# Performance work log

Hardware: AMD Instinct MI355X
Metric: run time of the kernel (lower is better)

The kernel has to match this reference:

```python
import jax, jax.numpy as jnp
import numpy as np

B, S, D, H = 2, 2048, 1024, 16
HD = D // H  # 64


def rotate_half(x):
    x1, x2 = x[..., : x.shape[-1] // 2], x[..., x.shape[-1] // 2 :]
    return jnp.concatenate((-x2, x1), axis=-1)


def setup_inputs() -> dict:
    key = jax.random.key(0)
    ks = jax.random.split(key, 8)
    return {
        "hidden_states": jax.random.normal(ks[0], (B, S, D), jnp.float32),
        "attention_bias": jax.random.normal(ks[1], (B, 1, S, S), jnp.float32),
        "cos": jax.random.uniform(ks[2], (1, S, 1, HD), jnp.float32),
        "sin": jax.random.uniform(ks[3], (1, S, 1, HD), jnp.float32),
        "Wqkv": jax.random.normal(ks[4], (D, 3 * D), jnp.float32) * (D ** -0.5),
        "bqkv": jnp.zeros((3 * D,), jnp.float32),
        "Wo": jax.random.normal(ks[5], (D, D), jnp.float32) * (D ** -0.5),
        "bo": jnp.zeros((D,), jnp.float32),
    }


def reference(hidden_states, attention_bias, cos, sin, Wqkv, bqkv, Wo, bo):
    # packed QKV projection: [B,S,D] -> [B,S,3D]
    qkv = hidden_states @ Wqkv + bqkv
    q, k, v = jnp.split(qkv, 3, axis=-1)
    # reshape to [B,S,H,HD]
    q = q.reshape(B, S, H, HD)
    k = k.reshape(B, S, H, HD)
    v = v.reshape(B, S, H, HD)
    # rotary position embedding
    q = q * cos + rotate_half(q) * sin
    k = k * cos + rotate_half(k) * sin
    # scaled dot-product attention with additive bias
    scores = jnp.einsum("bqhd,bkhd->bhqk", q, k) / jnp.sqrt(jnp.float32(HD))
    scores = scores + attention_bias
    probs = jax.nn.softmax(scores, axis=-1)
    ctx = jnp.einsum("bhqk,bkhd->bqhd", probs, v)  # [B,S,H,HD]
    ctx = ctx.reshape(B, S, D)
    return ctx @ Wo + bo
```

## Files before the change

### kernel.cpp

```cpp
#include <hip/hip_runtime.h>
#include <stdint.h>

typedef unsigned short u16;
typedef __attribute__((ext_vector_type(8))) short short8;
typedef __attribute__((ext_vector_type(4))) float f32x4;

#define DI __device__ __forceinline__

constexpr int S_LEN = 2048;
constexpr float LOG2E = 1.44269504088896f;
constexpr float SC = 0.125f * 1.44269504088896f;

DI float bf2f(u16 u) { union { uint32_t i; float f; } v; v.i = ((uint32_t)u) << 16; return v.f; }
DI u16 f2bf(float f) {
  union { float f; uint32_t i; } v; v.f = f;
  return (u16)((v.i + 0x7FFFu + ((v.i >> 16) & 1u)) >> 16);
}
DI uint32_t cvtpk(float lo, float hi) {
  uint32_t r;
  asm("v_cvt_pk_bf16_f32 %0, %1, %2" : "=v"(r) : "v"(lo), "v"(hi));
  return r;
}
DI float exp2r(float x) {
  float r;
  asm("v_exp_f32 %0, %1" : "=v"(r) : "v"(x));
  return r;
}

DI void cp16(const void* g, void* l) {
  auto gp = reinterpret_cast<const __attribute__((address_space(1))) uint32_t*>(
      reinterpret_cast<uintptr_t>(g));
  auto lp = reinterpret_cast<__attribute__((address_space(3))) uint32_t*>(
      reinterpret_cast<uintptr_t>(l));
  __builtin_amdgcn_global_load_lds(gp, lp, 16, 0, 0);
}

DI f32x4 mfma16(short8 a, short8 b, f32x4 c) {
  return __builtin_amdgcn_mfma_f32_16x16x32_bf16(a, b, c, 0, 0, 0);
}

DI int permk(int rl) {
  return ((rl >> 5) & 1) * 32 + ((rl >> 2) & 3) * 8 + ((rl >> 4) & 1) * 4 + (rl & 3);
}

__global__ __launch_bounds__(256) void k_cvt(const float* __restrict__ in,
                                             u16* __restrict__ out, int n4) {
  int i = blockIdx.x * 256 + threadIdx.x;
  if (i >= n4) return;
  float4 v = ((const float4*)in)[i];
  ushort4 o = { f2bf(v.x), f2bf(v.y), f2bf(v.z), f2bf(v.w) };
  ((ushort4*)out)[i] = o;
}

__global__ __launch_bounds__(256) void k_cvtb(const float* __restrict__ in,
                                              u16* __restrict__ out, int n4) {
  int i = blockIdx.x * 256 + threadIdx.x;
  if (i >= n4) return;
  float4 v = ((const float4*)in)[i];
  ushort4 o = { f2bf(v.x * LOG2E), f2bf(v.y * LOG2E), f2bf(v.z * LOG2E), f2bf(v.w * LOG2E) };
  ((ushort4*)out)[i] = o;
}

__global__ __launch_bounds__(256) void k_tr(const float* __restrict__ in,
                                            u16* __restrict__ out, int R, int C) {
  __shared__ float t[32][33];
  int tx = threadIdx.x & 31, ty = threadIdx.x >> 5;
  int c0 = blockIdx.x * 32, r0 = blockIdx.y * 32;
#pragma unroll
  for (int k = 0; k < 4; k++)
    t[ty + 8 * k][tx] = in[(size_t)(r0 + ty + 8 * k) * C + c0 + tx];
  __syncthreads();
#pragma unroll
  for (int k = 0; k < 4; k++)
    out[(size_t)(c0 + ty + 8 * k) * R + r0 + tx] = f2bf(t[tx][ty + 8 * k]);
}

template <int STORE_F32>
__global__ __launch_bounds__(256) void k_gemm(const u16* __restrict__ A,
                                              const u16* __restrict__ Bt,
                                              const float* __restrict__ bias,
                                              void* __restrict__ Cout,
                                              int N, int K, int nbx) {
  __shared__ u16 Al[128 * 32];
  __shared__ u16 Bl[128 * 32];
  int nwg = gridDim.x;
  int per = nwg >> 3;
  int id = blockIdx.x;
  int sid = (id & 7) * per + (id >> 3);
  int bx = sid % nbx, by = sid / nbx;
  int row0 = by * 128, col0 = bx * 128;
  int tid = threadIdx.x;
  int lane = tid & 63, wave = tid >> 6;
  int lg = lane >> 4, lc = lane & 15;
  int wr = wave >> 1, wc = wave & 1;
  int srow = tid >> 2, sseg = tid & 3;
  const u16* ga = A + (size_t)(row0 + srow) * K + sseg * 8;
  const u16* gb = Bt + (size_t)(col0 + srow) * K + sseg * 8;
  u16* la = Al + tid * 8;
  u16* lb = Bl + tid * 8;
  size_t half = (size_t)64 * K;
  f32x4 acc[4][4] = {};
  for (int ko = 0; ko < K; ko += 32) {
    cp16(ga + ko, la);
    cp16(ga + ko + half, la + 2048);
    cp16(gb + ko, lb);
    cp16(gb + ko + half, lb + 2048);
    __syncthreads();
    short8 af[4], bf[4];
#pragma unroll
    for (int i = 0; i < 4; i++)
      af[i] = *(const short8*)&Al[(wr * 64 + i * 16 + lc) * 32 + lg * 8];
#pragma unroll
    for (int j = 0; j < 4; j++)
      bf[j] = *(const short8*)&Bl[(wc * 64 + j * 16 + lc) * 32 + lg * 8];
#pragma unroll
    for (int i = 0; i < 4; i++)
#pragma unroll
      for (int j = 0; j < 4; j++) acc[i][j] = mfma16(af[i], bf[j], acc[i][j]);
    __syncthreads();
  }
#pragma unroll
  for (int i = 0; i < 4; i++) {
    int r = row0 + wr * 64 + i * 16 + lg * 4;
#pragma unroll
    for (int j = 0; j < 4; j++) {
      int c = col0 + wc * 64 + j * 16 + lc;
      float bv = bias[c];
#pragma unroll
      for (int q = 0; q < 4; q++) {
        float v = acc[i][j][q] + bv;
        if constexpr (STORE_F32)
          ((float*)Cout)[(size_t)(r + q) * N + c] = v;
        else
          ((u16*)Cout)[(size_t)(r + q) * N + c] = f2bf(v);
      }
    }
  }
}

__global__ __launch_bounds__(256) void k_rope(u16* __restrict__ qkv,
                                              const float* __restrict__ cosb,
                                              const float* __restrict__ sinb) {
  int idx = blockIdx.x * 256 + threadIdx.x;
  int d = idx & 31;
  int h = (idx >> 5) & 15;
  int s = (idx >> 9) & 2047;
  int b = idx >> 20;
  size_t base = (size_t)(b * S_LEN + s) * 3072 + h * 64 + d;
  float c1 = cosb[s * 64 + d], s1 = sinb[s * 64 + d];
  float c2 = cosb[s * 64 + d + 32], s2 = sinb[s * 64 + d + 32];
  float x1 = bf2f(qkv[base]), x2 = bf2f(qkv[base + 32]);
  qkv[base] = f2bf(x1 * c1 - x2 * s1);
  qkv[base + 32] = f2bf(x2 * c2 + x1 * s2);
  float y1 = bf2f(qkv[base + 1024]), y2 = bf2f(qkv[base + 1056]);
  qkv[base + 1024] = f2bf(y1 * c1 - y2 * s1);
  qkv[base + 1056] = f2bf(y2 * c2 + y1 * s2);
}

__global__ __launch_bounds__(256) void k_vtrans(const u16* __restrict__ qkv,
                                                u16* __restrict__ vtg) {
  __shared__ u16 Vl[64 * 66];
  int bh = blockIdx.y, b = bh >> 4, h = bh & 15;
  int s0 = blockIdx.x * 64;
  int tid = threadIdx.x;
  int r = tid >> 3, seg = tid & 7;
  const u16* src = qkv + (size_t)(b * S_LEN + s0) * 3072 + 2048 + h * 64 + seg * 8;
#pragma unroll
  for (int p = 0; p < 2; p++) {
    int s = r + 32 * p;
    short8 v = *(const short8*)(src + (size_t)s * 3072);
    const uint32_t* vw = (const uint32_t*)&v;
    uint32_t* dst = (uint32_t*)&Vl[s * 66 + seg * 8];
#pragma unroll
    for (int q = 0; q < 4; q++) dst[q] = vw[q];
  }
  __syncthreads();
  u16* out = vtg + (size_t)bh * 64 * 2048 + s0 + seg * 8;
#pragma unroll
  for (int p = 0; p < 2; p++) {
    int d = r + 32 * p;
    short8 o;
#pragma unroll
    for (int j = 0; j < 8; j++) o[j] = (short)Vl[(seg * 8 + j) * 66 + d];
    *(short8*)(out + (size_t)d * 2048) = o;
  }
}

DI float sm_pa(const f32x4 st[4], const short8* bc, short8 pa[2]) {
  float acc = 0.f;
  uint32_t w[4][2];
#pragma unroll
  for (int j = 0; j < 4; j++) {
    int base = (j & 1) * 4;
    float b0 = bf2f((u16)(j < 2 ? bc[0][base + 0] : bc[1][base + 0]));
    float b1 = bf2f((u16)(j < 2 ? bc[0][base + 1] : bc[1][base + 1]));
    float b2 = bf2f((u16)(j < 2 ? bc[0][base + 2] : bc[1][base + 2]));
    float b3 = bf2f((u16)(j < 2 ? bc[0][base + 3] : bc[1][base + 3]));
    float e0 = exp2r(st[j][0] * SC + b0);
    float e1 = exp2r(st[j][1] * SC + b1);
    float e2 = exp2r(st[j][2] * SC + b2);
    float e3 = exp2r(st[j][3] * SC + b3);
    acc += (e0 + e1) + (e2 + e3);
    w[j][0] = cvtpk(e0, e1);
    w[j][1] = cvtpk(e2, e3);
  }
  union { short8 s; uint32_t u[4]; } p0, p1;
  p0.u[0] = w[0][0]; p0.u[1] = w[0][1]; p0.u[2] = w[1][0]; p0.u[3] = w[1][1];
  p1.u[0] = w[2][0]; p1.u[1] = w[2][1]; p1.u[2] = w[3][0]; p1.u[3] = w[3][1];
  pa[0] = p0.s;
  pa[1] = p1.s;
  return acc;
}

DI void attn_store(u16* __restrict__ ctx, const f32x4 o[4], float lsumT,
                   size_t rowbase, int hcol, int lg, int lc) {
  float rinv[4];
#pragma unroll
  for (int r = 0; r < 4; r++) rinv[r] = 1.0f / __shfl(lsumT, lg * 4 + r);
#pragma unroll
  for (int j = 0; j < 4; j++)
#pragma unroll
    for (int r = 0; r < 4; r++)
      ctx[(rowbase + lg * 4 + r) * 1024 + hcol + j * 16 + lc] =
          f2bf(o[j][r] * rinv[r]);
}

__global__ __launch_bounds__(256, 2) void k_attn(const u16* __restrict__ qkv,
                                                 const u16* __restrict__ biasl2,
                                                 const u16* __restrict__ vtg,
                                                 u16* __restrict__ ctx) {
  __shared__ u16 Kl[2][4096];
  __shared__ u16 Vl[2][4096];
  constexpr int nkt = 32;
  int id = blockIdx.x;
  int idx = id >> 3;
  int bh = (id & 7) * 4 + (idx & 3);
  int qt = idx >> 2;
  int b = bh >> 4, h = bh & 15;
  int tid = threadIdx.x, lane = tid & 63, wave = tid >> 6;
  int lg = lane >> 4, lc = lane & 15;
  int q0 = qt * 128 + wave * 32;

  const u16* qb = qkv + (size_t)(b * S_LEN + q0 + lc) * 3072 + h * 64 + lg * 8;
  short8 qf[2][2];
#pragma unroll
  for (int s = 0; s < 2; s++) {
    qf[s][0] = *(const short8*)(qb + (size_t)s * 16 * 3072);
    qf[s][1] = *(const short8*)(qb + (size_t)s * 16 * 3072 + 32);
  }

  int srow = tid >> 3, sseg = tid & 7;
  const u16* kst[2];
  const u16* vst[2];
#pragma unroll
  for (int p = 0; p < 2; p++) {
    int rl = srow + 32 * p;
    int sw = (sseg ^ (rl & 7)) * 8;
    kst[p] = qkv + (size_t)(b * S_LEN + permk(rl)) * 3072 + 1024 + h * 64 + sw;
    vst[p] = vtg + (size_t)bh * 64 * 2048 + (size_t)rl * 2048 + sw;
  }

  const u16* bp0 = biasl2 + ((size_t)b * S_LEN + q0 + lc) * 2048 + lg * 8;
  const u16* bp1 = bp0 + (size_t)16 * 2048;

  f32x4 o0[4] = {}, o1[4] = {};
  float lsum0 = 0.f, lsum1 = 0.f;

#pragma unroll
  for (int p = 0; p < 2; p++) {
    cp16(kst[p], (u16*)&Kl[0][0] + p * 2048 + tid * 8);
    cp16(vst[p], (u16*)&Vl[0][0] + p * 2048 + tid * 8);
    kst[p] += (size_t)64 * 3072;
    vst[p] += 64;
  }
  short8 bA[4], bB[4];
  bA[0] = *(const short8*)bp0;
  bA[1] = *(const short8*)(bp0 + 32);
  bA[2] = *(const short8*)bp1;
  bA[3] = *(const short8*)(bp1 + 32);
  bp0 += 64;
  bp1 += 64;
  __syncthreads();

  auto tile = [&](int kt, int cur, const short8* bc, short8* bn) {
    if (kt < nkt - 1) {
#pragma unroll
      for (int p = 0; p < 2; p++) {
        cp16(kst[p], (u16*)&Kl[cur ^ 1][0] + p * 2048 + tid * 8);
        cp16(vst[p], (u16*)&Vl[cur ^ 1][0] + p * 2048 + tid * 8);
        kst[p] += (size_t)64 * 3072;
        vst[p] += 64;
      }
      bn[0] = *(const short8*)bp0;
      bn[1] = *(const short8*)(bp0 + 32);
      bn[2] = *(const short8*)bp1;
      bn[3] = *(const short8*)(bp1 + 32);
      bp0 += 64;
      bp1 += 64;
    }
    f32x4 st0[4] = {}, st1[4] = {};
    __builtin_amdgcn_s_setprio(1);
#pragma unroll
    for (int kk = 0; kk < 2; kk++) {
      short8 kf[4];
#pragma unroll
      for (int j = 0; j < 4; j++) {
        int row = j * 16 + lc;
        kf[j] = *(const short8*)&Kl[cur][row * 64 + (((kk * 4 + lg) ^ (row & 7)) * 8)];
      }
#pragma unroll
      for (int j = 0; j < 4; j++) {
        st0[j] = mfma16(kf[j], qf[0][kk], st0[j]);
        st1[j] = mfma16(kf[j], qf[1][kk], st1[j]);
      }
    }
    __builtin_amdgcn_s_setprio(0);
    short8 pa0[2], pa1[2];
    lsum0 += sm_pa(st0, bc, pa0);
    lsum1 += sm_pa(st1, bc + 2, pa1);
    __builtin_amdgcn_s_setprio(1);
#pragma unroll
    for (int kk = 0; kk < 2; kk++) {
      short8 vf[4];
#pragma unroll
      for (int j = 0; j < 4; j++) {
        int row = j * 16 + lc;
        vf[j] = *(const short8*)&Vl[cur][row * 64 + (((kk * 4 + lg) ^ (row & 7)) * 8)];
      }
#pragma unroll
      for (int j = 0; j < 4; j++) {
        o0[j] = mfma16(pa0[kk], vf[j], o0[j]);
        o1[j] = mfma16(pa1[kk], vf[j], o1[j]);
      }
    }
    __builtin_amdgcn_s_setprio(0);
    __syncthreads();
  };

  for (int kt = 0; kt < nkt; kt += 2) {
    tile(kt, 0, bA, bB);
    tile(kt + 1, 1, bB, bA);
  }

  float t0 = lsum0;
  t0 += __shfl_xor(t0, 16);
  t0 += __shfl_xor(t0, 32);
  float t1 = lsum1;
  t1 += __shfl_xor(t1, 16);
  t1 += __shfl_xor(t1, 32);
  size_t rowbase = (size_t)b * S_LEN + q0;
  attn_store(ctx, o0, t0, rowbase, h * 64, lg, lc);
  attn_store(ctx, o1, t1, rowbase + 16, h * 64, lg, lc);
}

extern "C" void kernel_launch(void* const* d_in, const int* in_sizes, int n_in,
                              void* d_out, int out_size, void* d_ws, size_t ws_size,
                              hipStream_t stream) {
  (void)in_sizes; (void)n_in; (void)out_size; (void)ws_size;
  const float* hs   = (const float*)d_in[0];
  const float* bias = (const float*)d_in[1];
  const float* cosb = (const float*)d_in[2];
  const float* sinb = (const float*)d_in[3];
  const float* Wqkv = (const float*)d_in[4];
  const float* bqkv = (const float*)d_in[5];
  const float* Wo   = (const float*)d_in[6];
  const float* bo   = (const float*)d_in[7];
  float* out = (float*)d_out;
  char* ws = (char*)d_ws;
  u16* h_bf   = (u16*)(ws + 0);
  u16* wqkvT  = (u16*)(ws + 8388608);
  u16* woT    = (u16*)(ws + 14680064);
  u16* biasbf = (u16*)(ws + 16777216);
  u16* qkv    = (u16*)(ws + 33554432);
  u16* vtg    = (u16*)(ws + 58720256);
  u16* ctxb   = (u16*)(ws + 67108864);

  k_cvt<<<4096, 256, 0, stream>>>(hs, h_bf, 1048576);
  k_cvtb<<<8192, 256, 0, stream>>>(bias, biasbf, 2097152);
  k_tr<<<dim3(96, 32), 256, 0, stream>>>(Wqkv, wqkvT, 1024, 3072);
  k_tr<<<dim3(32, 32), 256, 0, stream>>>(Wo, woT, 1024, 1024);
  k_gemm<0><<<768, 256, 0, stream>>>(h_bf, wqkvT, bqkv, qkv, 3072, 1024, 24);
  k_rope<<<8192, 256, 0, stream>>>(qkv, cosb, sinb);
  k_vtrans<<<dim3(32, 32), 256, 0, stream>>>(qkv, vtg);
  k_attn<<<512, 256, 0, stream>>>(qkv, biasbf, vtg, ctxb);
  k_gemm<1><<<256, 256, 0, stream>>>(ctxb, woT, bo, out, 1024, 1024, 8);
}
```

Baseline: 159.7 us.

## Fuse RoPE into QKV GEMM epilogue and halve attention query tile

Rotary embedding for the Q and K columns now runs inside the QKV GEMM epilogue. This drops the separate k_rope kernel and its read-modify-write pass over the bf16 qkv buffer, and applies RoPE to f32 values before the bf16 rounding. The attention kernel now gives each wave 16 query rows instead of 32. That doubles the grid to 1024 blocks and raises the launch-bounds occupancy hint from 2 to 4, to increase parallelism and cut register pressure. The cost is that each K/V tile staged in LDS is reused by half as many query rows, which doubles K/V traffic from global memory and L2.

```diff
diff --git a/kernel.cpp b/kernel.cpp
--- a/kernel.cpp
+++ b/kernel.cpp
@@ -75,11 +75,13 @@
     out[(size_t)(c0 + ty + 8 * k) * R + r0 + tx] = f2bf(t[tx][ty + 8 * k]);
 }
 
-template <int STORE_F32>
+template <int STORE_F32, int ROPE>
 __global__ __launch_bounds__(256) void k_gemm(const u16* __restrict__ A,
                                               const u16* __restrict__ Bt,
                                               const float* __restrict__ bias,
                                               void* __restrict__ Cout,
+                                              const float* __restrict__ cosb,
+                                              const float* __restrict__ sinb,
                                               int N, int K, int nbx) {
   __shared__ u16 Al[128 * 32];
   __shared__ u16 Bl[128 * 32];
@@ -119,42 +121,42 @@
       for (int j = 0; j < 4; j++) acc[i][j] = mfma16(af[i], bf[j], acc[i][j]);
     __syncthreads();
   }
+  int cbase = col0 + wc * 64 + lc;
+  float bv[4];
+#pragma unroll
+  for (int j = 0; j < 4; j++) bv[j] = bias[cbase + j * 16];
+  bool do_rope = false;
+  if constexpr (ROPE) do_rope = (col0 < 2048);
 #pragma unroll
   for (int i = 0; i < 4; i++) {
     int r = row0 + wr * 64 + i * 16 + lg * 4;
 #pragma unroll
-    for (int j = 0; j < 4; j++) {
-      int c = col0 + wc * 64 + j * 16 + lc;
-      float bv = bias[c];
-#pragma unroll
-      for (int q = 0; q < 4; q++) {
-        float v = acc[i][j][q] + bv;
+    for (int q = 0; q < 4; q++) {
+      float v[4];
+#pragma unroll
+      for (int j = 0; j < 4; j++) v[j] = acc[i][j][q] + bv[j];
+      if (do_rope) {
+        int s = (r + q) & 2047;
+        const float* cb = cosb + s * 64 + lc;
+        const float* sb = sinb + s * 64 + lc;
+#pragma unroll
+        for (int jp = 0; jp < 2; jp++) {
+          float cl = cb[jp * 16], sl = sb[jp * 16];
+          float ch = cb[jp * 16 + 32], sh = sb[jp * 16 + 32];
+          float x1 = v[jp], x2 = v[jp + 2];
+          v[jp] = x1 * cl - x2 * sl;
+          v[jp + 2] = x2 * ch + x1 * sh;
+        }
+      }
+#pragma unroll
+      for (int j = 0; j < 4; j++) {
         if constexpr (STORE_F32)
-          ((float*)Cout)[(size_t)(r + q) * N + c] = v;
+          ((float*)Cout)[(size_t)(r + q) * N + cbase + j * 16] = v[j];
         else
-          ((u16*)Cout)[(size_t)(r + q) * N + c] = f2bf(v);
+          ((u16*)Cout)[(size_t)(r + q) * N + cbase + j * 16] = f2bf(v[j]);
       }
     }
   }
-}
-
-__global__ __launch_bounds__(256) void k_rope(u16* __restrict__ qkv,
-                                              const float* __restrict__ cosb,
-                                              const float* __restrict__ sinb) {
-  int idx = blockIdx.x * 256 + threadIdx.x;
-  int d = idx & 31;
-  int h = (idx >> 5) & 15;
-  int s = (idx >> 9) & 2047;
-  int b = idx >> 20;
-  size_t base = (size_t)(b * S_LEN + s) * 3072 + h * 64 + d;
-  float c1 = cosb[s * 64 + d], s1 = sinb[s * 64 + d];
-  float c2 = cosb[s * 64 + d + 32], s2 = sinb[s * 64 + d + 32];
-  float x1 = bf2f(qkv[base]), x2 = bf2f(qkv[base + 32]);
-  qkv[base] = f2bf(x1 * c1 - x2 * s1);
-  qkv[base + 32] = f2bf(x2 * c2 + x1 * s2);
-  float y1 = bf2f(qkv[base + 1024]), y2 = bf2f(qkv[base + 1056]);
-  qkv[base + 1024] = f2bf(y1 * c1 - y2 * s1);
-  qkv[base + 1056] = f2bf(y2 * c2 + y1 * s2);
 }
 
 __global__ __launch_bounds__(256) void k_vtrans(const u16* __restrict__ qkv,
@@ -225,7 +227,7 @@
           f2bf(o[j][r] * rinv[r]);
 }
 
-__global__ __launch_bounds__(256, 2) void k_attn(const u16* __restrict__ qkv,
+__global__ __launch_bounds__(256, 4) void k_attn(const u16* __restrict__ qkv,
                                                  const u16* __restrict__ biasl2,
                                                  const u16* __restrict__ vtg,
                                                  u16* __restrict__ ctx) {
@@ -239,15 +241,11 @@
   int b = bh >> 4, h = bh & 15;
   int tid = threadIdx.x, lane = tid & 63, wave = tid >> 6;
   int lg = lane >> 4, lc = lane & 15;
-  int q0 = qt * 128 + wave * 32;
+  int q0 = qt * 64 + wave * 16;
 
   const u16* qb = qkv + (size_t)(b * S_LEN + q0 + lc) * 3072 + h * 64 + lg * 8;
-  short8 qf[2][2];
-#pragma unroll
-  for (int s = 0; s < 2; s++) {
-    qf[s][0] = *(const short8*)(qb + (size_t)s * 16 * 3072);
-    qf[s][1] = *(const short8*)(qb + (size_t)s * 16 * 3072 + 32);
-  }
+  short8 qf0 = *(const short8*)qb;
+  short8 qf1 = *(const short8*)(qb + 32);
 
   int srow = tid >> 3, sseg = tid & 7;
   const u16* kst[2];
@@ -260,11 +258,10 @@
     vst[p] = vtg + (size_t)bh * 64 * 2048 + (size_t)rl * 2048 + sw;
   }
 
-  const u16* bp0 = biasl2 + ((size_t)b * S_LEN + q0 + lc) * 2048 + lg * 8;
-  const u16* bp1 = bp0 + (size_t)16 * 2048;
-
-  f32x4 o0[4] = {}, o1[4] = {};
-  float lsum0 = 0.f, lsum1 = 0.f;
+  const u16* bp = biasl2 + ((size_t)b * S_LEN + q0 + lc) * 2048 + lg * 8;
+
+  f32x4 o[4] = {};
+  float lsum = 0.f;
 
 #pragma unroll
   for (int p = 0; p < 2; p++) {
@@ -273,13 +270,10 @@
     kst[p] += (size_t)64 * 3072;
     vst[p] += 64;
   }
-  short8 bA[4], bB[4];
-  bA[0] = *(const short8*)bp0;
-  bA[1] = *(const short8*)(bp0 + 32);
-  bA[2] = *(const short8*)bp1;
-  bA[3] = *(const short8*)(bp1 + 32);
-  bp0 += 64;
-  bp1 += 64;
+  short8 bA[2], bB[2];
+  bA[0] = *(const short8*)bp;
+  bA[1] = *(const short8*)(bp + 32);
+  bp += 64;
   __syncthreads();
 
   auto tile = [&](int kt, int cur, const short8* bc, short8* bn) {
@@ -291,46 +285,33 @@
         kst[p] += (size_t)64 * 3072;
         vst[p] += 64;
       }
-      bn[0] = *(const short8*)bp0;
-      bn[1] = *(const short8*)(bp0 + 32);
-      bn[2] = *(const short8*)bp1;
-      bn[3] = *(const short8*)(bp1 + 32);
-      bp0 += 64;
-      bp1 += 64;
+      bn[0] = *(const short8*)bp;
+      bn[1] = *(const short8*)(bp + 32);
+      bp += 64;
     }
-    f32x4 st0[4] = {}, st1[4] = {};
+    f32x4 st[4] = {};
     __builtin_amdgcn_s_setprio(1);
 #pragma unroll
     for (int kk = 0; kk < 2; kk++) {
-      short8 kf[4];
+      short8 qa = kk ? qf1 : qf0;
 #pragma unroll
       for (int j = 0; j < 4; j++) {
         int row = j * 16 + lc;
-        kf[j] = *(const short8*)&Kl[cur][row * 64 + (((kk * 4 + lg) ^ (row & 7)) * 8)];
-      }
-#pragma unroll
-      for (int j = 0; j < 4; j++) {
-        st0[j] = mfma16(kf[j], qf[0][kk], st0[j]);
-        st1[j] = mfma16(kf[j], qf[1][kk], st1[j]);
+        short8 kf = *(const short8*)&Kl[cur][row * 64 + (((kk * 4 + lg) ^ (row & 7)) * 8)];
+        st[j] = mfma16(kf, qa, st[j]);
       }
     }
     __builtin_amdgcn_s_setprio(0);
-    short8 pa0[2], pa1[2];
-    lsum0 += sm_pa(st0, bc, pa0);
-    lsum1 += sm_pa(st1, bc + 2, pa1);
+    short8 pa[2];
+    lsum += sm_pa(st, bc, pa);
     __builtin_amdgcn_s_setprio(1);
 #pragma unroll
     for (int kk = 0; kk < 2; kk++) {
-      short8 vf[4];
 #pragma unroll
       for (int j = 0; j < 4; j++) {
         int row = j * 16 + lc;
-        vf[j] = *(const short8*)&Vl[cur][row * 64 + (((kk * 4 + lg) ^ (row & 7)) * 8)];
-      }
-#pragma unroll
-      for (int j = 0; j < 4; j++) {
-        o0[j] = mfma16(pa0[kk], vf[j], o0[j]);
-        o1[j] = mfma16(pa1[kk], vf[j], o1[j]);
+        short8 vf = *(const short8*)&Vl[cur][row * 64 + (((kk * 4 + lg) ^ (row & 7)) * 8)];
+        o[j] = mfma16(pa[kk], vf, o[j]);
       }
     }
     __builtin_amdgcn_s_setprio(0);
@@ -342,15 +323,10 @@
     tile(kt + 1, 1, bB, bA);
   }
 
-  float t0 = lsum0;
+  float t0 = lsum;
   t0 += __shfl_xor(t0, 16);
   t0 += __shfl_xor(t0, 32);
-  float t1 = lsum1;
-  t1 += __shfl_xor(t1, 16);
-  t1 += __shfl_xor(t1, 32);
-  size_t rowbase = (size_t)b * S_LEN + q0;
-  attn_store(ctx, o0, t0, rowbase, h * 64, lg, lc);
-  attn_store(ctx, o1, t1, rowbase + 16, h * 64, lg, lc);
+  attn_store(ctx, o, t0, (size_t)b * S_LEN + q0, h * 64, lg, lc);
 }
 
 extern "C" void kernel_launch(void* const* d_in, const int* in_sizes, int n_in,
@@ -379,9 +355,10 @@
   k_cvtb<<<8192, 256, 0, stream>>>(bias, biasbf, 2097152);
   k_tr<<<dim3(96, 32), 256, 0, stream>>>(Wqkv, wqkvT, 1024, 3072);
   k_tr<<<dim3(32, 32), 256, 0, stream>>>(Wo, woT, 1024, 1024);
-  k_gemm<0><<<768, 256, 0, stream>>>(h_bf, wqkvT, bqkv, qkv, 3072, 1024, 24);
-  k_rope<<<8192, 256, 0, stream>>>(qkv, cosb, sinb);
+  k_gemm<0, 1><<<768, 256, 0, stream>>>(h_bf, wqkvT, bqkv, qkv, cosb, sinb,
+                                        3072, 1024, 24);
   k_vtrans<<<dim3(32, 32), 256, 0, stream>>>(qkv, vtg);
-  k_attn<<<512, 256, 0, stream>>>(qkv, biasbf, vtg, ctxb);
-  k_gemm<1><<<256, 256, 0, stream>>>(ctxb, woT, bo, out, 1024, 1024, 8);
-}
+  k_attn<<<1024, 256, 0, stream>>>(qkv, biasbf, vtg, ctxb);
+  k_gemm<1, 0><<<256, 256, 0, stream>>>(ctxb, woT, bo, out, nullptr, nullptr,
+                                        1024, 1024, 8);
+}
```

New measurement: 156.7 us. About the same (-1.9%).
